# Performance work log

Measured on AMD Instinct MI355X. Metric: run time of the kernel, lower is better.

Reference implementation:

```python
import jax, jax.numpy as jnp
import numpy as np

B, T, D = 8, 2048, 1024  # batch, seq (== block_size), n_embd == head_size


def setup_inputs() -> dict:
    key = jax.random.key(0)
    k0, k1, k2, k3 = jax.random.split(key, 4)
    s = 1.0 / np.sqrt(D)
    return {
        "x": jax.random.normal(k0, (B, T, D), dtype=jnp.float32),
        "Wk": jax.random.normal(k1, (D, D), dtype=jnp.float32) * s,
        "Wq": jax.random.normal(k2, (D, D), dtype=jnp.float32) * s,
        "Wv": jax.random.normal(k3, (D, D), dtype=jnp.float32) * s,
    }


def reference(x, Wk, Wq, Wv):
    Bb, Tt, C = x.shape
    k = jnp.einsum("btc,ch->bth", x, Wk)
    q = jnp.einsum("btc,ch->bth", x, Wq)
    v = jnp.einsum("btc,ch->bth", x, Wv)
    # scaled dot-product scores with causal (tril) mask; scale = C**-0.5 (n_embd)
    wei = jnp.einsum("bqh,bkh->bqk", q, k) * (1.0 / jnp.sqrt(jnp.float32(C)))
    causal = jnp.tril(jnp.ones((Tt, Tt), dtype=bool))
    wei = jnp.where(causal[None, :, :], wei, jnp.float32(-jnp.inf))
    wei = jax.nn.softmax(wei, axis=-1)
    # dropout is identity in eval mode
    out = jnp.einsum("bqk,bkh->bqh", wei, v)
    return out
```

## Files before the change

### kernel.cpp

```cpp
#include <hip/hip_runtime.h>
#include <hip/hip_bf16.h>

#define BB 8
#define TT 2048
#define DD 1024

typedef __attribute__((ext_vector_type(8))) short short8;
typedef __attribute__((ext_vector_type(4))) float f32x4;
typedef __attribute__((ext_vector_type(4))) unsigned short u16x4;

__device__ inline void gload_lds16(const void* g, void* l) {
    __builtin_amdgcn_global_load_lds((const __attribute__((address_space(1))) void*)g,
                                     (__attribute__((address_space(3))) void*)l, 16, 0, 0);
}

template<int MODE, typename CT>
__device__ __forceinline__ void gemm_core(
    const __hip_bfloat16* __restrict__ A,
    const __hip_bfloat16* __restrict__ Bt,
    void* __restrict__ Cbase,
    int lda, int ldb, int ldc,
    int m0, int n0, int kmax,
    float scale, float* __restrict__ rs)
{
    __shared__ __align__(16) __hip_bfloat16 lsA[128 * 64];
    __shared__ __align__(16) __hip_bfloat16 lsB[128 * 64];

    const int t    = threadIdx.x;
    const int w    = t >> 6;
    const int l    = t & 63;
    const int quad = l >> 4;
    const int l16  = l & 15;
    const int wy   = w >> 1;
    const int wx   = w & 1;

    f32x4 acc[4][4];
#pragma unroll
    for (int i = 0; i < 4; i++)
#pragma unroll
        for (int j = 0; j < 4; j++) acc[i][j] = f32x4{0.f, 0.f, 0.f, 0.f};

    for (int k0 = 0; k0 < kmax; k0 += 64) {
#pragma unroll
        for (int p = 0; p < 4; p++) {
            int c   = p * 256 + t;
            int row = c >> 3;
            int gch = (c & 7) ^ (row & 7);
            const __hip_bfloat16* ga = A  + (size_t)(m0 + row) * lda + (k0 + gch * 8);
            const __hip_bfloat16* gb = Bt + (size_t)(n0 + row) * ldb + (k0 + gch * 8);
            char* la = (char*)lsA + p * 4096 + w * 1024;
            char* lb = (char*)lsB + p * 4096 + w * 1024;
            gload_lds16(ga, la);
            gload_lds16(gb, lb);
        }
        __syncthreads();

#pragma unroll
        for (int h = 0; h < 2; h++) {
            short8 aF[4], bF[4];
#pragma unroll
            for (int mf = 0; mf < 4; mf++) {
                int m = wy * 64 + mf * 16 + l16;
                aF[mf] = *(const short8*)((const char*)lsA + m * 128 +
                                          (((h * 4 + quad) ^ (m & 7)) * 16));
            }
#pragma unroll
            for (int nf = 0; nf < 4; nf++) {
                int n = wx * 64 + nf * 16 + l16;
                bF[nf] = *(const short8*)((const char*)lsB + n * 128 +
                                          (((h * 4 + quad) ^ (n & 7)) * 16));
            }
#pragma unroll
            for (int mf = 0; mf < 4; mf++)
#pragma unroll
                for (int nf = 0; nf < 4; nf++)
                    acc[mf][nf] = __builtin_amdgcn_mfma_f32_16x16x32_bf16(
                        aF[mf], bF[nf], acc[mf][nf], 0, 0, 0);
        }
        __syncthreads();
    }

    if constexpr (MODE == 0) {
        CT* C = (CT*)Cbase;
#pragma unroll
        for (int mf = 0; mf < 4; mf++) {
            int rbase = m0 + wy * 64 + mf * 16 + quad * 4;
#pragma unroll
            for (int nf = 0; nf < 4; nf++) {
                int col = n0 + wx * 64 + nf * 16 + l16;
#pragma unroll
                for (int r = 0; r < 4; r++) {
                    float v = acc[mf][nf][r] * scale;
                    if constexpr (sizeof(CT) == 2)
                        C[(size_t)(rbase + r) * ldc + col] = (CT)__float2bfloat16(v);
                    else
                        *((float*)&C[(size_t)(rbase + r) * ldc + col]) = v;
                }
            }
        }
    } else if constexpr (MODE == 1) {
        __hip_bfloat16* C = (__hip_bfloat16*)Cbase;
#pragma unroll
        for (int mf = 0; mf < 4; mf++) {
            int rbase = m0 + wy * 64 + mf * 16 + quad * 4;
#pragma unroll
            for (int r = 0; r < 4; r++) {
                int row = rbase + r;
                float part = 0.f, pv[4];
#pragma unroll
                for (int nf = 0; nf < 4; nf++) {
                    int col = n0 + wx * 64 + nf * 16 + l16;
                    float e = (col <= row) ? __expf(acc[mf][nf][r] * scale) : 0.f;
                    pv[nf] = e;
                    part += e;
                }
                part += __shfl_xor(part, 1, 64);
                part += __shfl_xor(part, 2, 64);
                part += __shfl_xor(part, 4, 64);
                part += __shfl_xor(part, 8, 64);
                if (l16 == 0) atomicAdd(&rs[row], part);
#pragma unroll
                for (int nf = 0; nf < 4; nf++) {
                    int col = n0 + wx * 64 + nf * 16 + l16;
                    C[(size_t)row * ldc + col] = __float2bfloat16(pv[nf]);
                }
            }
        }
    } else {
        float* C = (float*)Cbase;
#pragma unroll
        for (int mf = 0; mf < 4; mf++) {
            int rbase = m0 + wy * 64 + mf * 16 + quad * 4;
#pragma unroll
            for (int r = 0; r < 4; r++) {
                int row = rbase + r;
                float inv = 1.f / rs[row];
#pragma unroll
                for (int nf = 0; nf < 4; nf++) {
                    int col = n0 + wx * 64 + nf * 16 + l16;
                    C[(size_t)row * ldc + col] = acc[mf][nf][r] * inv;
                }
            }
        }
    }
}

__global__ __launch_bounds__(256, 4) void proj3(
    const __hip_bfloat16* __restrict__ xb,
    const __hip_bfloat16* __restrict__ wt,
    __hip_bfloat16* __restrict__ kq,
    __hip_bfloat16* __restrict__ vT2)
{
    const int z = blockIdx.z;
    const __hip_bfloat16 *A, *Bt;
    void* C;
    int ldc, m0, n0;
    if (z < 2) {
        A = xb; Bt = wt + z * 1048576; C = kq + (size_t)z * 16777216;
        ldc = 1024; m0 = blockIdx.x * 128; n0 = blockIdx.y * 128;
    } else {
        A = wt + 2 * 1048576; Bt = xb; C = vT2;
        ldc = 16384; m0 = blockIdx.y * 128; n0 = blockIdx.x * 128;
    }
    gemm_core<0, __hip_bfloat16>(A, Bt, C, 1024, 1024, ldc, m0, n0, 1024, 1.0f, nullptr);
}

template<int MODE, typename CT>
__global__ __launch_bounds__(256, 4) void gemm_bt(
    const __hip_bfloat16* __restrict__ Abase,
    const __hip_bfloat16* __restrict__ Btbase,
    void* __restrict__ Cbase,
    int K, int lda, int ldb, int ldc,
    long long sA, long long sB, long long sC,
    float scale, int causalSkip, int causalKStop, int swapMN, int permX,
    float* __restrict__ aux)
{
    int bx = blockIdx.x;
    if (permX) bx = (bx < 8) ? 15 - bx : bx - 8;
    const int m0 = (swapMN ? bx : blockIdx.y) * 128;
    const int n0 = (swapMN ? blockIdx.y : bx) * 128;
    if (causalSkip && n0 > m0) return;

    const int z = blockIdx.z;
    int kmax = K;
    if (causalKStop) { int km = m0 + 128; kmax = km < K ? km : K; }

    gemm_core<MODE, CT>(Abase + (size_t)z * sA, Btbase + (size_t)z * sB,
                        (char*)Cbase + (size_t)z * sC * sizeof(CT),
                        lda, ldb, ldc, m0, n0, kmax, scale,
                        aux ? aux + (size_t)z * TT : nullptr);
}

__global__ __launch_bounds__(256) void cvt_x(const float* __restrict__ in,
                                             unsigned short* __restrict__ out)
{
    size_t i = ((size_t)blockIdx.x * 256 + threadIdx.x) * 4;
    float4 f = *(const float4*)(in + i);
    union { u16x4 u; __hip_bfloat16 h[4]; } o;
    o.h[0] = __float2bfloat16(f.x);
    o.h[1] = __float2bfloat16(f.y);
    o.h[2] = __float2bfloat16(f.z);
    o.h[3] = __float2bfloat16(f.w);
    *(u16x4*)(out + i) = o.u;
}

__global__ __launch_bounds__(256) void transpose_cvt_w(
    const float* __restrict__ Wk, const float* __restrict__ Wq,
    const float* __restrict__ Wv, __hip_bfloat16* __restrict__ Wt)
{
    const float* W = blockIdx.z == 0 ? Wk : (blockIdx.z == 1 ? Wq : Wv);
    __hip_bfloat16* o = Wt + (size_t)blockIdx.z * DD * DD;
    int h0 = blockIdx.x * 32, c0 = blockIdx.y * 32;
    __shared__ float tl[32][33];
    int tx = threadIdx.x, ty = threadIdx.y;
#pragma unroll
    for (int k = 0; k < 4; k++)
        tl[ty + 8 * k][tx] = W[(size_t)(c0 + ty + 8 * k) * DD + h0 + tx];
    __syncthreads();
#pragma unroll
    for (int k = 0; k < 4; k++)
        o[(size_t)(h0 + ty + 8 * k) * DD + c0 + tx] = __float2bfloat16(tl[tx][ty + 8 * k]);
}

extern "C" void kernel_launch(void* const* d_in, const int* in_sizes, int n_in,
                              void* d_out, int out_size, void* d_ws, size_t ws_size,
                              hipStream_t stream)
{
    const float* x  = (const float*)d_in[0];
    const float* Wk = (const float*)d_in[1];
    const float* Wq = (const float*)d_in[2];
    const float* Wv = (const float*)d_in[3];
    float* out = (float*)d_out;

    char* ws = (char*)d_ws;
    __hip_bfloat16* kk   = (__hip_bfloat16*)ws;
    __hip_bfloat16* qq   = (__hip_bfloat16*)(ws + 33554432);
    __hip_bfloat16* vT2  = (__hip_bfloat16*)(ws + 67108864);
    __hip_bfloat16* wt   = (__hip_bfloat16*)(ws + 100663296);
    float*          rsum = (float*)         (ws + 100663296);
    __hip_bfloat16* xb   = (__hip_bfloat16*)(ws + 106954752);
    __hip_bfloat16* Pp   = (__hip_bfloat16*)(ws + 106954752);

    int g = (ws_size >= 106954752ull + 8ull * 8388608ull) ? 8 : 4;

    cvt_x<<<16384, 256, 0, stream>>>(x, (unsigned short*)xb);
    transpose_cvt_w<<<dim3(32, 32, 3), dim3(32, 8), 0, stream>>>(Wk, Wq, Wv, wt);

    proj3<<<dim3(128, 8, 3), 256, 0, stream>>>(xb, wt, kk, vT2);

    for (int g0 = 0; g0 < BB; g0 += g) {
        hipMemsetAsync(rsum, 0, (size_t)g * TT * 4, stream);

        gemm_bt<1, __hip_bfloat16><<<dim3(16, 16, g), 256, 0, stream>>>(
            qq + (size_t)g0 * 2097152, kk + (size_t)g0 * 2097152, (void*)Pp,
            1024, 1024, 1024, 2048,
            2097152LL, 2097152LL, 4194304LL, 0.03125f, 1, 0, 0, 1, rsum);

        gemm_bt<2, float><<<dim3(16, 8, g), 256, 0, stream>>>(
            Pp, vT2 + (size_t)g0 * 2048, (void*)(out + (size_t)g0 * 2097152),
            2048, 2048, 16384, 1024,
            4194304LL, 2048LL, 2097152LL, 1.0f, 0, 1, 1, 1, rsum);
    }
}
```

Before: 360.6 us.

## Pack causal score tiles into triangular tiled buffer and launch only needed blocks

Replaces the full 16x16 grid of score-GEMM blocks, of which about half exited immediately, with a compact 136-block launch that maps each block index to a lower-triangular tile (y,x). The P matrix is stored as contiguous 128x128 tiles in a packed triangular layout, which halves the workspace needed and lets the PV GEMM read P tile-by-tile through a packed-A addressing mode. This aims to remove wasted block launches and shrink P memory traffic and footprint, which may also allow all 8 batches to be processed in one group. The tau interleaving spreads heavy and light tiles across the grid, but the per-block triangular index computation with sqrt adds some overhead.

```diff
diff --git a/kernel.cpp b/kernel.cpp
--- a/kernel.cpp
+++ b/kernel.cpp
@@ -14,7 +14,7 @@
                                      (__attribute__((address_space(3))) void*)l, 16, 0, 0);
 }
 
-template<int MODE, typename CT>
+template<int MODE, typename CT, bool TILEC, bool PACKA>
 __device__ __forceinline__ void gemm_core(
     const __hip_bfloat16* __restrict__ A,
     const __hip_bfloat16* __restrict__ Bt,
@@ -46,7 +46,12 @@
             int c   = p * 256 + t;
             int row = c >> 3;
             int gch = (c & 7) ^ (row & 7);
-            const __hip_bfloat16* ga = A  + (size_t)(m0 + row) * lda + (k0 + gch * 8);
+            const __hip_bfloat16* ga;
+            if constexpr (PACKA)
+                ga = A + ((size_t)(k0 >> 7) << 14) + row * 128 +
+                     ((k0 & 127) + gch * 8);
+            else
+                ga = A + (size_t)(m0 + row) * lda + (k0 + gch * 8);
             const __hip_bfloat16* gb = Bt + (size_t)(n0 + row) * ldb + (k0 + gch * 8);
             char* la = (char*)lsA + p * 4096 + w * 1024;
             char* lb = (char*)lsB + p * 4096 + w * 1024;
@@ -102,14 +107,16 @@
         __hip_bfloat16* C = (__hip_bfloat16*)Cbase;
 #pragma unroll
         for (int mf = 0; mf < 4; mf++) {
-            int rbase = m0 + wy * 64 + mf * 16 + quad * 4;
+            int lrb = wy * 64 + mf * 16 + quad * 4;
 #pragma unroll
             for (int r = 0; r < 4; r++) {
-                int row = rbase + r;
+                int lr  = lrb + r;
+                int row = m0 + lr;
                 float part = 0.f, pv[4];
 #pragma unroll
                 for (int nf = 0; nf < 4; nf++) {
-                    int col = n0 + wx * 64 + nf * 16 + l16;
+                    int lc  = wx * 64 + nf * 16 + l16;
+                    int col = n0 + lc;
                     float e = (col <= row) ? __expf(acc[mf][nf][r] * scale) : 0.f;
                     pv[nf] = e;
                     part += e;
@@ -121,8 +128,11 @@
                 if (l16 == 0) atomicAdd(&rs[row], part);
 #pragma unroll
                 for (int nf = 0; nf < 4; nf++) {
-                    int col = n0 + wx * 64 + nf * 16 + l16;
-                    C[(size_t)row * ldc + col] = __float2bfloat16(pv[nf]);
+                    int lc = wx * 64 + nf * 16 + l16;
+                    if constexpr (TILEC)
+                        C[lr * 128 + lc] = __float2bfloat16(pv[nf]);
+                    else
+                        C[(size_t)(m0 + lr) * ldc + (n0 + lc)] = __float2bfloat16(pv[nf]);
                 }
             }
         }
@@ -162,33 +172,44 @@
         A = wt + 2 * 1048576; Bt = xb; C = vT2;
         ldc = 16384; m0 = blockIdx.y * 128; n0 = blockIdx.x * 128;
     }
-    gemm_core<0, __hip_bfloat16>(A, Bt, C, 1024, 1024, ldc, m0, n0, 1024, 1.0f, nullptr);
-}
-
-template<int MODE, typename CT>
-__global__ __launch_bounds__(256, 4) void gemm_bt(
-    const __hip_bfloat16* __restrict__ Abase,
-    const __hip_bfloat16* __restrict__ Btbase,
-    void* __restrict__ Cbase,
-    int K, int lda, int ldb, int ldc,
-    long long sA, long long sB, long long sC,
-    float scale, int causalSkip, int causalKStop, int swapMN, int permX,
-    float* __restrict__ aux)
+    gemm_core<0, __hip_bfloat16, false, false>(A, Bt, C, 1024, 1024, ldc,
+                                               m0, n0, 1024, 1.0f, nullptr);
+}
+
+__global__ __launch_bounds__(256, 4) void sgemm_pk(
+    const __hip_bfloat16* __restrict__ qq,
+    const __hip_bfloat16* __restrict__ kk,
+    __hip_bfloat16* __restrict__ Pp,
+    float* __restrict__ rsum)
+{
+    const int tau = (blockIdx.x & 7) * 17 + (blockIdx.x >> 3);
+    int y = (int)((sqrtf(8.f * tau + 1.f) - 1.f) * 0.5f);
+    while ((y + 1) * (y + 2) / 2 <= tau) ++y;
+    while (y * (y + 1) / 2 > tau) --y;
+    const int x = tau - y * (y + 1) / 2;
+    const int z = blockIdx.z;
+    gemm_core<1, __hip_bfloat16, true, false>(
+        qq + (size_t)z * 2097152, kk + (size_t)z * 2097152,
+        Pp + (size_t)z * 2228224 + (size_t)tau * 16384,
+        1024, 1024, 128, y * 128, x * 128, 1024, 0.03125f,
+        rsum + (size_t)z * TT);
+}
+
+__global__ __launch_bounds__(256, 4) void pvgemm_pk(
+    const __hip_bfloat16* __restrict__ Pp,
+    const __hip_bfloat16* __restrict__ vT2,
+    float* __restrict__ out,
+    float* __restrict__ rsum)
 {
     int bx = blockIdx.x;
-    if (permX) bx = (bx < 8) ? 15 - bx : bx - 8;
-    const int m0 = (swapMN ? bx : blockIdx.y) * 128;
-    const int n0 = (swapMN ? blockIdx.y : bx) * 128;
-    if (causalSkip && n0 > m0) return;
-
+    const int y = (bx < 8) ? 15 - bx : bx - 8;
     const int z = blockIdx.z;
-    int kmax = K;
-    if (causalKStop) { int km = m0 + 128; kmax = km < K ? km : K; }
-
-    gemm_core<MODE, CT>(Abase + (size_t)z * sA, Btbase + (size_t)z * sB,
-                        (char*)Cbase + (size_t)z * sC * sizeof(CT),
-                        lda, ldb, ldc, m0, n0, kmax, scale,
-                        aux ? aux + (size_t)z * TT : nullptr);
+    const __hip_bfloat16* A = Pp + (size_t)z * 2228224 +
+                              (size_t)(y * (y + 1) / 2) * 16384;
+    gemm_core<2, float, false, true>(
+        A, vT2 + (size_t)z * 2048, out + (size_t)z * 2097152,
+        0, 16384, 1024, y * 128, blockIdx.y * 128, (y + 1) * 128, 1.0f,
+        rsum + (size_t)z * TT);
 }
 
 __global__ __launch_bounds__(256) void cvt_x(const float* __restrict__ in,
@@ -241,7 +262,7 @@
     __hip_bfloat16* xb   = (__hip_bfloat16*)(ws + 106954752);
     __hip_bfloat16* Pp   = (__hip_bfloat16*)(ws + 106954752);
 
-    int g = (ws_size >= 106954752ull + 8ull * 8388608ull) ? 8 : 4;
+    int g = (ws_size >= 106954752ull + 8ull * 4456448ull) ? 8 : 4;
 
     cvt_x<<<16384, 256, 0, stream>>>(x, (unsigned short*)xb);
     transpose_cvt_w<<<dim3(32, 32, 3), dim3(32, 8), 0, stream>>>(Wk, Wq, Wv, wt);
@@ -251,14 +272,10 @@
     for (int g0 = 0; g0 < BB; g0 += g) {
         hipMemsetAsync(rsum, 0, (size_t)g * TT * 4, stream);
 
-        gemm_bt<1, __hip_bfloat16><<<dim3(16, 16, g), 256, 0, stream>>>(
-            qq + (size_t)g0 * 2097152, kk + (size_t)g0 * 2097152, (void*)Pp,
-            1024, 1024, 1024, 2048,
-            2097152LL, 2097152LL, 4194304LL, 0.03125f, 1, 0, 0, 1, rsum);
-
-        gemm_bt<2, float><<<dim3(16, 8, g), 256, 0, stream>>>(
-            Pp, vT2 + (size_t)g0 * 2048, (void*)(out + (size_t)g0 * 2097152),
-            2048, 2048, 16384, 1024,
-            4194304LL, 2048LL, 2097152LL, 1.0f, 0, 1, 1, 1, rsum);
-    }
-}
+        sgemm_pk<<<dim3(136, 1, g), 256, 0, stream>>>(
+            qq + (size_t)g0 * 2097152, kk + (size_t)g0 * 2097152, Pp, rsum);
+
+        pvgemm_pk<<<dim3(16, 8, g), 256, 0, stream>>>(
+            Pp, vT2 + (size_t)g0 * 2048, out + (size_t)g0 * 2097152, rsum);
+    }
+}
```

After: 356.8 us. No clear change (-1.1%).
